# Optimization experiments

Measured on AMD Instinct MI355X. Metric: run time of the kernel, lower is better.

The kernel has to match this reference:

```python
import jax, jax.numpy as jnp
import numpy as np

D_IN = 2048
H1 = D_IN // 4      # 512
H2 = D_IN // 16     # 128
N_EXP = 8
N_CLS = 10
BATCH = 16384


def setup_inputs() -> dict:
    key = jax.random.key(0)
    ks = jax.random.split(key, 16)
    s = lambda k, shape, fan_in: jax.random.normal(k, shape, jnp.float32) / np.sqrt(fan_in)
    return {
        "fs": jax.random.normal(ks[0], (BATCH, D_IN // 2), jnp.float32),
        "fp": jax.random.normal(ks[1], (BATCH, D_IN // 2), jnp.float32),
        # gate MLP params (output = num_source, softmax)
        "gW1": s(ks[2], (D_IN, H1), D_IN), "gb1": jnp.zeros((H1,), jnp.float32),
        "gW2": s(ks[3], (H1, H2), H1),     "gb2": jnp.zeros((H2,), jnp.float32),
        "gW3": s(ks[4], (H2, N_EXP), H2), "gb3": jnp.zeros((N_EXP,), jnp.float32),
        # stacked expert MLP params (output = num classes, log_softmax)
        "eW1": s(ks[5], (N_EXP, D_IN, H1), D_IN), "eb1": jnp.zeros((N_EXP, H1), jnp.float32),
        "eW2": s(ks[6], (N_EXP, H1, H2), H1),     "eb2": jnp.zeros((N_EXP, H2), jnp.float32),
        "eW3": s(ks[7], (N_EXP, H2, N_CLS), H2),  "eb3": jnp.zeros((N_EXP, N_CLS), jnp.float32),
    }


def reference(fs, fp, gW1, gb1, gW2, gb2, gW3, gb3, eW1, eb1, eW2, eb2, eW3, eb3):
    features = jnp.concatenate([fs, fp], axis=-1)            # [B, D_IN]

    # Gate MLP on detached features (detach is a no-op for fwd), softmax output
    g = jax.nn.relu(features @ gW1 + gb1)
    g = jax.nn.relu(g @ gW2 + gb2)
    gate_outs = jax.nn.softmax(g @ gW3 + gb3, axis=-1)       # [B, E]

    # All experts as batched GEMMs over stacked weights, log_softmax output
    h = jax.nn.relu(jnp.einsum('bd,edh->beh', features, eW1) + eb1[None])   # [B, E, H1]
    h = jax.nn.relu(jnp.einsum('beh,ehk->bek', h, eW2) + eb2[None])         # [B, E, H2]
    logits = jnp.einsum('bek,eko->beo', h, eW3) + eb3[None]                 # [B, E, C]
    expert_outs = jax.nn.log_softmax(logits, axis=-1)                       # [B, E, C]

    # Gate-weighted sum over experts
    output = jnp.einsum('be,bec->bc', gate_outs, expert_outs)               # [B, C]
    return output, gate_outs
```

## Files before the change

kernel.cpp:

```cpp
#include <hip/hip_runtime.h>
#include <hip/hip_bf16.h>

#define B_SZ   16384
#define DIN    2048
#define H1_SZ  512
#define H2_SZ  128
#define N_EXP  8
#define N_CLS  10
#define N1     4608
#define N2     1152

typedef __attribute__((ext_vector_type(8))) __bf16 bf16x8;
typedef __attribute__((ext_vector_type(4))) float  floatx4;
typedef __attribute__((ext_vector_type(4))) short  short4v;
typedef __attribute__((ext_vector_type(8))) short  short8v;

__device__ __forceinline__ float bf2f(short s) {
  unsigned int u = ((unsigned int)(unsigned short)s) << 16;
  float f; __builtin_memcpy(&f, &u, 4); return f;
}

__global__ void convert_features_kernel(const float* __restrict__ fs,
                                        const float* __restrict__ fp,
                                        __hip_bfloat16* __restrict__ X) {
  const int nf4 = B_SZ * (DIN / 4);
  const float4* fs4 = (const float4*)fs;
  const float4* fp4 = (const float4*)fp;
  for (int i = blockIdx.x * blockDim.x + threadIdx.x; i < nf4;
       i += gridDim.x * blockDim.x) {
    int c = i & 511;
    int row = i >> 9;
    float4 v = (c < 256) ? fs4[(size_t)row * 256 + c]
                         : fp4[(size_t)row * 256 + (c - 256)];
    union { short4v v4; __hip_bfloat16 h[4]; } u;
    u.h[0] = __float2bfloat16(v.x);
    u.h[1] = __float2bfloat16(v.y);
    u.h[2] = __float2bfloat16(v.z);
    u.h[3] = __float2bfloat16(v.w);
    *(short4v*)(X + (size_t)i * 4) = u.v4;
  }
}

__global__ void transpose_convert_kernel(const float* __restrict__ expert_src,
                                         const float* __restrict__ gate_src,
                                         int K, int H, int E,
                                         __hip_bfloat16* __restrict__ out) {
  __shared__ float t[32][33];
  int k0 = blockIdx.x * 32;
  int n0 = blockIdx.y * 32;
  int e = n0 / H;
  const float* src; int h0;
  if (e < E) { src = expert_src + (size_t)e * K * H; h0 = n0 - e * H; }
  else       { src = gate_src;                       h0 = n0 - E * H; }
  int tx = threadIdx.x, ty = threadIdx.y;
  #pragma unroll
  for (int j = 0; j < 4; ++j) {
    int r = ty + j * 8;
    t[r][tx] = src[(size_t)(k0 + r) * H + h0 + tx];
  }
  __syncthreads();
  #pragma unroll
  for (int j = 0; j < 4; ++j) {
    int r = ty + j * 8;
    out[(size_t)(n0 + r) * K + k0 + tx] = __float2bfloat16(t[tx][r]);
  }
}

__device__ __forceinline__ void stage_sub(
    const __hip_bfloat16* __restrict__ src, int ld, int row0, int kofs,
    __hip_bfloat16* dst, int tid) {
  #pragma unroll
  for (int j = 0; j < 2; ++j) {
    int c = j * 512 + tid;
    int r = c >> 2;
    int cl = (c & 3) ^ ((r >> 1) & 3);
    __builtin_amdgcn_global_load_lds(
        (const __attribute__((address_space(1))) unsigned int*)(
            src + (size_t)(row0 + r) * ld + kofs + cl * 8),
        (__attribute__((address_space(3))) unsigned int*)(dst + c * 8),
        16, 0, 0);
  }
}

__device__ __forceinline__ bf16x8 ldsfrag(const __hip_bfloat16* sub, int r, int lquad) {
  int slot = lquad ^ ((r >> 1) & 3);
  return *(const bf16x8*)(sub + r * 32 + slot * 8);
}

template <bool RDB, int MH>
__device__ __forceinline__ void phase8(
    const __hip_bfloat16* Asub, const __hip_bfloat16* Bsub,
    floatx4 (&acc)[8][4], bf16x8 (&b)[4],
    int wm, int wn, int lrow, int lquad,
    const __hip_bfloat16* __restrict__ ssrc, int sld, int srow0, int skofs,
    __hip_bfloat16* sdst, int tid) {
  bf16x8 a[4];
  #pragma unroll
  for (int q = 0; q < 4; ++q)
    a[q] = ldsfrag(Asub, wm + (MH * 4 + q) * 16 + lrow, lquad);
  if (RDB) {
    #pragma unroll
    for (int nt = 0; nt < 4; ++nt)
      b[nt] = ldsfrag(Bsub, wn + nt * 16 + lrow, lquad);
  }
  stage_sub(ssrc, sld, srow0, skofs, sdst, tid);
  asm volatile("s_waitcnt vmcnt(8)" ::: "memory");
  __builtin_amdgcn_s_barrier();
  __builtin_amdgcn_s_setprio(1);
  #pragma unroll
  for (int q = 0; q < 4; ++q)
    #pragma unroll
    for (int nt = 0; nt < 4; ++nt)
      acc[MH * 4 + q][nt] = __builtin_amdgcn_mfma_f32_16x16x32_bf16(
          a[q], b[nt], acc[MH * 4 + q][nt], 0, 0, 0);
  __builtin_amdgcn_s_setprio(0);
  asm volatile("s_waitcnt lgkmcnt(0)" ::: "memory");
  __builtin_amdgcn_s_barrier();
}

__global__ __launch_bounds__(512, 2) void gemm1_kernel8(
    const __hip_bfloat16* __restrict__ X, const __hip_bfloat16* __restrict__ W1T,
    const float* __restrict__ eb1, const float* __restrict__ gb1,
    __hip_bfloat16* __restrict__ H1) {
  __shared__ __align__(16) __hip_bfloat16 lds[8][256 * 32];

  const int tid  = threadIdx.x;
  const int lane = tid & 63;
  const int wave = tid >> 6;
  const int wm   = (wave >> 2) * 128;
  const int wn   = (wave & 3) * 64;
  const int lrow  = lane & 15;
  const int lquad = lane >> 4;

  int flat = blockIdx.x;
  int swz  = (flat & 7) * ((int)gridDim.x >> 3) + (flat >> 3);
  int m0 = (swz / (N1 / 256)) * 256;
  int n0 = (swz % (N1 / 256)) * 256;

  floatx4 acc[8][4] = {};
  bf16x8 b[4];

  const int KT = DIN / 64;

  stage_sub(X,   DIN, m0, 0,  lds[0], tid);
  stage_sub(W1T, DIN, n0, 0,  lds[2], tid);
  stage_sub(X,   DIN, m0, 32, lds[1], tid);
  stage_sub(W1T, DIN, n0, 32, lds[3], tid);
  stage_sub(X,   DIN, m0, 64, lds[4], tid);
  stage_sub(W1T, DIN, n0, 64, lds[6], tid);
  asm volatile("s_waitcnt vmcnt(8)" ::: "memory");
  __builtin_amdgcn_s_barrier();

  for (int i = 0; i < KT / 2; ++i) {
    int T  = 2 * i;
    int k1 = (T + 1) * 64;
    int k2 = min(T + 2, KT - 1) * 64;
    int k3 = min(T + 3, KT - 1) * 64;
    phase8<true,  0>(lds[0], lds[2], acc, b, wm, wn, lrow, lquad,
                     X,   DIN, m0, k1 + 32, lds[5], tid);
    phase8<false, 1>(lds[0], lds[2], acc, b, wm, wn, lrow, lquad,
                     W1T, DIN, n0, k1 + 32, lds[7], tid);
    phase8<true,  0>(lds[1], lds[3], acc, b, wm, wn, lrow, lquad,
                     X,   DIN, m0, k2,      lds[0], tid);
    phase8<false, 1>(lds[1], lds[3], acc, b, wm, wn, lrow, lquad,
                     W1T, DIN, n0, k2,      lds[2], tid);
    phase8<true,  0>(lds[4], lds[6], acc, b, wm, wn, lrow, lquad,
                     X,   DIN, m0, k2 + 32, lds[1], tid);
    phase8<false, 1>(lds[4], lds[6], acc, b, wm, wn, lrow, lquad,
                     W1T, DIN, n0, k2 + 32, lds[3], tid);
    phase8<true,  0>(lds[5], lds[7], acc, b, wm, wn, lrow, lquad,
                     X,   DIN, m0, k3,      lds[4], tid);
    phase8<false, 1>(lds[5], lds[7], acc, b, wm, wn, lrow, lquad,
                     W1T, DIN, n0, k3,      lds[6], tid);
  }

  const float* bias = (n0 < N_EXP * H1_SZ) ? (eb1 + n0) : (gb1 + (n0 - N_EXP * H1_SZ));
  #pragma unroll
  for (int nt = 0; nt < 4; ++nt) {
    int col = wn + nt * 16 + lrow;
    float bv = bias[col];
    #pragma unroll
    for (int mt = 0; mt < 8; ++mt) {
      #pragma unroll
      for (int r = 0; r < 4; ++r) {
        int row = m0 + wm + mt * 16 + lquad * 4 + r;
        float v = acc[mt][nt][r] + bv;
        v = v > 0.f ? v : 0.f;
        H1[(size_t)row * N1 + n0 + col] = __float2bfloat16(v);
      }
    }
  }
}

__device__ __forceinline__ void gemm_core(
    const __hip_bfloat16* __restrict__ A,  int lda,
    const __hip_bfloat16* __restrict__ BT, int K,
    const float* __restrict__ bias,
    __hip_bfloat16* __restrict__ O, int ldo) {
  __shared__ __align__(16) __hip_bfloat16 As[128 * 64];
  __shared__ __align__(16) __hip_bfloat16 Bs[128 * 64];

  const int tid  = threadIdx.x;
  const int lane = tid & 63;
  const int wave = tid >> 6;
  const int wm   = (wave >> 1) * 64;
  const int wn   = (wave & 1) * 64;
  const int lrow  = lane & 15;
  const int lquad = lane >> 4;

  floatx4 acc[4][4] = {};

  for (int k0 = 0; k0 < K; k0 += 64) {
    #pragma unroll
    for (int j = 0; j < 4; ++j) {
      int chunk = j * 256 + tid;
      int mi = chunk >> 3;
      int cs = chunk & 7;
      int cl = cs ^ (mi & 7);
      __builtin_amdgcn_global_load_lds(
          (const __attribute__((address_space(1))) unsigned int*)(A + (size_t)mi * lda + k0 + cl * 8),
          (__attribute__((address_space(3))) unsigned int*)(As + chunk * 8),
          16, 0, 0);
      __builtin_amdgcn_global_load_lds(
          (const __attribute__((address_space(1))) unsigned int*)(BT + (size_t)mi * K + k0 + cl * 8),
          (__attribute__((address_space(3))) unsigned int*)(Bs + chunk * 8),
          16, 0, 0);
    }
    __syncthreads();
    #pragma unroll
    for (int ks = 0; ks < 2; ++ks) {
      bf16x8 a[4], b[4];
      #pragma unroll
      for (int t = 0; t < 4; ++t) {
        int ar = wm + t * 16 + lrow;
        int br = wn + t * 16 + lrow;
        int ca = (ks * 4 + lquad) ^ (ar & 7);
        int cb = (ks * 4 + lquad) ^ (br & 7);
        a[t] = *(const bf16x8*)(As + ar * 64 + ca * 8);
        b[t] = *(const bf16x8*)(Bs + br * 64 + cb * 8);
      }
      #pragma unroll
      for (int mt = 0; mt < 4; ++mt)
        #pragma unroll
        for (int nt = 0; nt < 4; ++nt)
          acc[mt][nt] = __builtin_amdgcn_mfma_f32_16x16x32_bf16(
              a[mt], b[nt], acc[mt][nt], 0, 0, 0);
    }
    __syncthreads();
  }

  #pragma unroll
  for (int nt = 0; nt < 4; ++nt) {
    int col = wn + nt * 16 + lrow;
    float bv = bias[col];
    #pragma unroll
    for (int mt = 0; mt < 4; ++mt) {
      #pragma unroll
      for (int r = 0; r < 4; ++r) {
        int row = wm + mt * 16 + lquad * 4 + r;
        float v = acc[mt][nt][r] + bv;
        v = v > 0.f ? v : 0.f;
        O[(size_t)row * ldo + col] = __float2bfloat16(v);
      }
    }
  }
}

__global__ __launch_bounds__(256, 2) void gemm2_kernel(
    const __hip_bfloat16* __restrict__ H1, const __hip_bfloat16* __restrict__ W2T,
    const float* __restrict__ eb2, const float* __restrict__ gb2,
    __hip_bfloat16* __restrict__ H2) {
  int m0 = blockIdx.y * 128;
  int z  = blockIdx.z;
  const float* bias = (z < N_EXP) ? (eb2 + z * H2_SZ) : gb2;
  gemm_core(H1 + (size_t)m0 * N1 + z * H1_SZ, N1,
            W2T + (size_t)z * H2_SZ * H1_SZ, H1_SZ,
            bias,
            H2 + (size_t)m0 * N2 + z * H2_SZ, N2);
}

__global__ __launch_bounds__(256) void layer3_kernel(
    const __hip_bfloat16* __restrict__ H2,
    const float* __restrict__ gW3, const float* __restrict__ gb3,
    const float* __restrict__ eW3, const float* __restrict__ eb3,
    float* __restrict__ out, float* __restrict__ gate_out) {
  int tid  = threadIdx.x;
  int j    = tid & 7;
  int rloc = tid >> 3;
  long row = (long)blockIdx.x * 32 + rloc;
  const __hip_bfloat16* hrow = H2 + row * N2;

  float accg = 0.f;
  float acc[N_CLS];
  #pragma unroll
  for (int c = 0; c < N_CLS; ++c) acc[c] = 0.f;

  #pragma unroll 4
  for (int k8 = 0; k8 < 16; ++k8) {
    short8v hg8 = *(const short8v*)(hrow + N_EXP * H2_SZ + k8 * 8);
    short8v he8 = *(const short8v*)(hrow + j * H2_SZ + k8 * 8);
    #pragma unroll
    for (int t = 0; t < 8; ++t) {
      int k = k8 * 8 + t;
      float hg = bf2f(hg8[t]);
      float he = bf2f(he8[t]);
      accg += hg * gW3[k * N_EXP + j];
      const float* w = eW3 + (size_t)(j * H2_SZ + k) * N_CLS;
      #pragma unroll
      for (int c = 0; c < N_CLS; ++c) acc[c] += he * w[c];
    }
  }

  float gj = accg + gb3[j];
  float mx = gj;
  mx = fmaxf(mx, __shfl_xor(mx, 1));
  mx = fmaxf(mx, __shfl_xor(mx, 2));
  mx = fmaxf(mx, __shfl_xor(mx, 4));
  float ex = __expf(gj - mx);
  float s = ex;
  s += __shfl_xor(s, 1);
  s += __shfl_xor(s, 2);
  s += __shfl_xor(s, 4);
  float gp = ex / s;

  float lg[N_CLS];
  float lm = -1e30f;
  #pragma unroll
  for (int c = 0; c < N_CLS; ++c) {
    lg[c] = acc[c] + eb3[j * N_CLS + c];
    lm = fmaxf(lm, lg[c]);
  }
  float es = 0.f;
  #pragma unroll
  for (int c = 0; c < N_CLS; ++c) es += __expf(lg[c] - lm);
  float lse = lm + __logf(es);

  float o[N_CLS];
  #pragma unroll
  for (int c = 0; c < N_CLS; ++c) o[c] = gp * (lg[c] - lse);
  #pragma unroll
  for (int c = 0; c < N_CLS; ++c) {
    o[c] += __shfl_xor(o[c], 1);
    o[c] += __shfl_xor(o[c], 2);
    o[c] += __shfl_xor(o[c], 4);
  }

  gate_out[row * N_EXP + j] = gp;
  if (j == 0) {
    #pragma unroll
    for (int c = 0; c < N_CLS; ++c) out[row * N_CLS + c] = o[c];
  }
}

extern "C" void kernel_launch(void* const* d_in, const int* in_sizes, int n_in,
                              void* d_out, int out_size, void* d_ws, size_t ws_size,
                              hipStream_t stream) {
  const float* fs  = (const float*)d_in[0];
  const float* fp  = (const float*)d_in[1];
  const float* gW1 = (const float*)d_in[2];
  const float* gb1 = (const float*)d_in[3];
  const float* gW2 = (const float*)d_in[4];
  const float* gb2 = (const float*)d_in[5];
  const float* gW3 = (const float*)d_in[6];
  const float* gb3 = (const float*)d_in[7];
  const float* eW1 = (const float*)d_in[8];
  const float* eb1 = (const float*)d_in[9];
  const float* eW2 = (const float*)d_in[10];
  const float* eb2 = (const float*)d_in[11];
  const float* eW3 = (const float*)d_in[12];
  const float* eb3 = (const float*)d_in[13];
  float* out = (float*)d_out;

  char* ws = (char*)d_ws;
  __hip_bfloat16* X   = (__hip_bfloat16*)ws;
  __hip_bfloat16* H2  = X;
  __hip_bfloat16* W1T = (__hip_bfloat16*)(ws + 67108864);
  __hip_bfloat16* W2T = (__hip_bfloat16*)(ws + 85983232);
  __hip_bfloat16* H1  = (__hip_bfloat16*)(ws + 87162880);

  convert_features_kernel<<<2048, 256, 0, stream>>>(fs, fp, X);
  transpose_convert_kernel<<<dim3(DIN / 32, N1 / 32), dim3(32, 8), 0, stream>>>(
      eW1, gW1, DIN, H1_SZ, N_EXP, W1T);
  transpose_convert_kernel<<<dim3(H1_SZ / 32, N2 / 32), dim3(32, 8), 0, stream>>>(
      eW2, gW2, H1_SZ, H2_SZ, N_EXP, W2T);
  gemm1_kernel8<<<dim3((N1 / 256) * (B_SZ / 256)), 512, 0, stream>>>(
      X, W1T, eb1, gb1, H1);
  gemm2_kernel<<<dim3(1, B_SZ / 128, N_EXP + 1), 256, 0, stream>>>(H1, W2T, eb2, gb2, H2);
  layer3_kernel<<<B_SZ / 32, 256, 0, stream>>>(H2, gW3, gb3, eW3, eb3,
                                               out, out + (size_t)B_SZ * N_CLS);
}
```

Measured before the change: 626.0 us.

## Software-pipeline LDS fragment loads one slot ahead of MFMAs in gemm1

Restructures the gemm1 main loop so each slot loads the next slot's A/B fragments from LDS into a second register set while the MFMAs run on the current set. It also drops one of the two barriers per slot, keeping a single waitcnt+barrier at the start. The aim is to hide LDS read latency behind matrix math and cut synchronisation. In exchange it doubles fragment register usage, which risks spills at 2 waves/SIMD occupancy, and the buffer reuse ordering is subtle and could race if the single barrier is not enough.

```diff
diff --git a/kernel.cpp b/kernel.cpp
--- a/kernel.cpp
+++ b/kernel.cpp
@@ -67,7 +67,7 @@
 }
 
 __device__ __forceinline__ void stage_sub(
-    const __hip_bfloat16* __restrict__ src, int ld, int row0, int kofs,
+    const __hip_bfloat16* __restrict__ src, int row0, int kofs,
     __hip_bfloat16* dst, int tid) {
   #pragma unroll
   for (int j = 0; j < 2; ++j) {
@@ -76,7 +76,7 @@
     int cl = (c & 3) ^ ((r >> 1) & 3);
     __builtin_amdgcn_global_load_lds(
         (const __attribute__((address_space(1))) unsigned int*)(
-            src + (size_t)(row0 + r) * ld + kofs + cl * 8),
+            src + (size_t)(row0 + r) * DIN + kofs + cl * 8),
         (__attribute__((address_space(3))) unsigned int*)(dst + c * 8),
         16, 0, 0);
   }
@@ -87,35 +87,34 @@
   return *(const bf16x8*)(sub + r * 32 + slot * 8);
 }
 
-template <bool RDB, int MH>
-__device__ __forceinline__ void phase8(
-    const __hip_bfloat16* Asub, const __hip_bfloat16* Bsub,
-    floatx4 (&acc)[8][4], bf16x8 (&b)[4],
+template <int MHC, int MHN, bool LOADB>
+__device__ __forceinline__ void pipe_slot(
+    floatx4 (&acc)[8][4],
+    bf16x8 (&a_cur)[4], bf16x8 (&b_cur)[4],
+    bf16x8 (&a_nxt)[4], bf16x8 (&b_nxt)[4],
+    const __hip_bfloat16* An, const __hip_bfloat16* Bn,
     int wm, int wn, int lrow, int lquad,
-    const __hip_bfloat16* __restrict__ ssrc, int sld, int srow0, int skofs,
+    const __hip_bfloat16* __restrict__ ssrc, int srow0, int skofs,
     __hip_bfloat16* sdst, int tid) {
-  bf16x8 a[4];
+  asm volatile("s_waitcnt vmcnt(6)\n\ts_barrier" ::: "memory");
   #pragma unroll
   for (int q = 0; q < 4; ++q)
-    a[q] = ldsfrag(Asub, wm + (MH * 4 + q) * 16 + lrow, lquad);
-  if (RDB) {
+    a_nxt[q] = ldsfrag(An, wm + (MHN * 4 + q) * 16 + lrow, lquad);
+  if (LOADB) {
     #pragma unroll
     for (int nt = 0; nt < 4; ++nt)
-      b[nt] = ldsfrag(Bsub, wn + nt * 16 + lrow, lquad);
-  }
-  stage_sub(ssrc, sld, srow0, skofs, sdst, tid);
-  asm volatile("s_waitcnt vmcnt(8)" ::: "memory");
-  __builtin_amdgcn_s_barrier();
+      b_nxt[nt] = ldsfrag(Bn, wn + nt * 16 + lrow, lquad);
+  }
+  stage_sub(ssrc, srow0, skofs, sdst, tid);
   __builtin_amdgcn_s_setprio(1);
   #pragma unroll
   for (int q = 0; q < 4; ++q)
     #pragma unroll
     for (int nt = 0; nt < 4; ++nt)
-      acc[MH * 4 + q][nt] = __builtin_amdgcn_mfma_f32_16x16x32_bf16(
-          a[q], b[nt], acc[MH * 4 + q][nt], 0, 0, 0);
+      acc[MHC * 4 + q][nt] = __builtin_amdgcn_mfma_f32_16x16x32_bf16(
+          a_cur[q], b_cur[nt], acc[MHC * 4 + q][nt], 0, 0, 0);
   __builtin_amdgcn_s_setprio(0);
   asm volatile("s_waitcnt lgkmcnt(0)" ::: "memory");
-  __builtin_amdgcn_s_barrier();
 }
 
 __global__ __launch_bounds__(512, 2) void gemm1_kernel8(
@@ -138,40 +137,46 @@
   int n0 = (swz % (N1 / 256)) * 256;
 
   floatx4 acc[8][4] = {};
-  bf16x8 b[4];
+  bf16x8 aX[4], aY[4], bX[4], bY[4];
 
   const int KT = DIN / 64;
 
-  stage_sub(X,   DIN, m0, 0,  lds[0], tid);
-  stage_sub(W1T, DIN, n0, 0,  lds[2], tid);
-  stage_sub(X,   DIN, m0, 32, lds[1], tid);
-  stage_sub(W1T, DIN, n0, 32, lds[3], tid);
-  stage_sub(X,   DIN, m0, 64, lds[4], tid);
-  stage_sub(W1T, DIN, n0, 64, lds[6], tid);
-  asm volatile("s_waitcnt vmcnt(8)" ::: "memory");
-  __builtin_amdgcn_s_barrier();
+  stage_sub(X,   m0, 0,  lds[0], tid);
+  stage_sub(W1T, n0, 0,  lds[2], tid);
+  stage_sub(X,   m0, 32, lds[1], tid);
+  stage_sub(W1T, n0, 32, lds[3], tid);
+  stage_sub(X,   m0, 64, lds[4], tid);
+  stage_sub(W1T, n0, 64, lds[6], tid);
+  asm volatile("s_waitcnt vmcnt(8)\n\ts_barrier" ::: "memory");
+  #pragma unroll
+  for (int q = 0; q < 4; ++q)
+    aX[q] = ldsfrag(lds[0], wm + q * 16 + lrow, lquad);
+  #pragma unroll
+  for (int nt = 0; nt < 4; ++nt)
+    bX[nt] = ldsfrag(lds[2], wn + nt * 16 + lrow, lquad);
+  asm volatile("s_waitcnt lgkmcnt(0)" ::: "memory");
 
   for (int i = 0; i < KT / 2; ++i) {
     int T  = 2 * i;
     int k1 = (T + 1) * 64;
     int k2 = min(T + 2, KT - 1) * 64;
     int k3 = min(T + 3, KT - 1) * 64;
-    phase8<true,  0>(lds[0], lds[2], acc, b, wm, wn, lrow, lquad,
-                     X,   DIN, m0, k1 + 32, lds[5], tid);
-    phase8<false, 1>(lds[0], lds[2], acc, b, wm, wn, lrow, lquad,
-                     W1T, DIN, n0, k1 + 32, lds[7], tid);
-    phase8<true,  0>(lds[1], lds[3], acc, b, wm, wn, lrow, lquad,
-                     X,   DIN, m0, k2,      lds[0], tid);
-    phase8<false, 1>(lds[1], lds[3], acc, b, wm, wn, lrow, lquad,
-                     W1T, DIN, n0, k2,      lds[2], tid);
-    phase8<true,  0>(lds[4], lds[6], acc, b, wm, wn, lrow, lquad,
-                     X,   DIN, m0, k2 + 32, lds[1], tid);
-    phase8<false, 1>(lds[4], lds[6], acc, b, wm, wn, lrow, lquad,
-                     W1T, DIN, n0, k2 + 32, lds[3], tid);
-    phase8<true,  0>(lds[5], lds[7], acc, b, wm, wn, lrow, lquad,
-                     X,   DIN, m0, k3,      lds[4], tid);
-    phase8<false, 1>(lds[5], lds[7], acc, b, wm, wn, lrow, lquad,
-                     W1T, DIN, n0, k3,      lds[6], tid);
+    pipe_slot<0,1,false>(acc, aX, bX, aY, bY, lds[0], lds[0],
+                         wm, wn, lrow, lquad, X,   m0, k1 + 32, lds[5], tid);
+    pipe_slot<1,0,true >(acc, aY, bX, aX, bY, lds[1], lds[3],
+                         wm, wn, lrow, lquad, W1T, n0, k1 + 32, lds[7], tid);
+    pipe_slot<0,1,false>(acc, aX, bY, aY, bX, lds[1], lds[1],
+                         wm, wn, lrow, lquad, X,   m0, k2,      lds[0], tid);
+    pipe_slot<1,0,true >(acc, aY, bY, aX, bX, lds[4], lds[6],
+                         wm, wn, lrow, lquad, W1T, n0, k2,      lds[2], tid);
+    pipe_slot<0,1,false>(acc, aX, bX, aY, bY, lds[4], lds[4],
+                         wm, wn, lrow, lquad, X,   m0, k2 + 32, lds[1], tid);
+    pipe_slot<1,0,true >(acc, aY, bX, aX, bY, lds[5], lds[7],
+                         wm, wn, lrow, lquad, W1T, n0, k2 + 32, lds[3], tid);
+    pipe_slot<0,1,false>(acc, aX, bY, aY, bX, lds[5], lds[5],
+                         wm, wn, lrow, lquad, X,   m0, k3,      lds[4], tid);
+    pipe_slot<1,0,true >(acc, aY, bY, aX, bX, lds[0], lds[2],
+                         wm, wn, lrow, lquad, W1T, n0, k3,      lds[6], tid);
   }
 
   const float* bias = (n0 < N_EXP * H1_SZ) ? (eb1 + n0) : (gb1 + (n0 - N_EXP * H1_SZ));
```

New measurement: 617.1 us. Within noise of the previous version (-1.4%).
